# Kernel optimization log

Hardware: AMD Instinct MI355X
Metric: run time of the kernel (lower is better)

Reference implementation:

```python
import jax, jax.numpy as jnp
import numpy as np

BINS = 256
MIN_V = -0.25
MAX_V = 1.25
XSIGMA = 1.0 / float(np.sqrt(2.0 * np.pi))
DELTA = (MAX_V - MIN_V) / BINS
SIGMA = DELTA * XSIGMA
# constant prefactor applied once to the joint kernel: delta / (sqrt(2*pi)*sigma)
COEF = float(DELTA / (np.sqrt(2.0 * np.pi) * SIGMA))

B, N = 8, 32768


def setup_inputs() -> dict:
    key = jax.random.key(0)
    k1, k2, k3 = jax.random.split(key, 3)
    x1 = jax.random.uniform(k1, (B, N), dtype=jnp.float32)
    x2 = jax.random.uniform(k2, (B, N), dtype=jnp.float32)
    mask = jax.random.uniform(k3, (B, N), dtype=jnp.float32)
    return {"x1": x1, "x2": x2, "mask": mask}


def reference(x1, x2, mask):
    # bin centers: (bins,)
    centers = MIN_V + DELTA * (jnp.arange(BINS, dtype=x1.dtype) + 0.5)
    inv_s = 1.0 / SIGMA
    # Separable factorization of exp(-0.5*((x1-ci)^2+(x2-cj)^2)/sigma^2):
    # g1: (b, bins, N), g2: (b, bins, N) with mask folded into g2.
    d1 = (x1[:, None, :] - centers[None, :, None]) * inv_s
    d2 = (x2[:, None, :] - centers[None, :, None]) * inv_s
    g1 = jnp.exp(-0.5 * d1 * d1)
    g2 = jnp.exp(-0.5 * d2 * d2) * mask[:, None, :]
    # contract over N via batched matmul -> (b, bins, bins)
    hist = jnp.einsum("bin,bjn->bij", g1, g2)
    return COEF * hist
```

## Files before the change

### kernel.cpp

```cpp
#include <hip/hip_runtime.h>


#define BINS   256
#define NPTS   32768
#define BATCH  8
#define TROWS  8
#define NTILE  (BINS / TROWS)

static constexpr float kInvDelta = 256.0f / 1.5f;
static constexpr float kUAdd     = 0.25f * (256.0f / 1.5f) - 0.5f;
static constexpr float kPi       = 3.14159265358979323846f;

__global__ __launch_bounds__(1024) void gh_gather(
    const float* __restrict__ x1, const float* __restrict__ x2,
    const float* __restrict__ mask, float* __restrict__ out)
{
    __shared__ float tile[TROWS * BINS];
    const int tid = threadIdx.x;
    const int r0  = blockIdx.x * TROWS;
    const int b   = blockIdx.y;

    for (int i = tid; i < TROWS * BINS; i += 1024) tile[i] = 0.0f;
    __syncthreads();

    const float4* X1 = (const float4*)(x1   + b * NPTS);
    const float4* X2 = (const float4*)(x2   + b * NPTS);
    const float4* M  = (const float4*)(mask + b * NPTS);

#pragma unroll 2
    for (int it = 0; it < NPTS / 4096; ++it) {
        const int n4 = it * 1024 + tid;
        const float4 a4 = X1[n4];
        const float4 b4 = X2[n4];
        const float4 m4 = M[n4];

        const float pv1[4] = {a4.x, a4.y, a4.z, a4.w};
        const float pv2[4] = {b4.x, b4.y, b4.z, b4.w};
        const float pm[4]  = {m4.x, m4.y, m4.z, m4.w};

#pragma unroll
        for (int k = 0; k < 4; ++k) {
            const float u1 = fmaf(pv1[k], kInvDelta, kUAdd);
            const float u2 = fmaf(pv2[k], kInvDelta, kUAdd);
            const float fi = rintf(u1);
            const float fj = rintf(u2);
            const int   i0 = (int)fi;
            int         j0 = (int)fj;
            j0 = min(254, max(1, j0));
            const float t1 = u1 - fi;
            const float t2 = u2 - (float)j0;

            float w1[3], w2[3];
#pragma unroll
            for (int a = 0; a < 3; ++a) {
                const float d1 = t1 - (float)(a - 1);
                const float d2 = t2 - (float)(a - 1);
                w1[a] = __expf(-kPi * d1 * d1);
                w2[a] = __expf(-kPi * d2 * d2) * pm[k];
            }

            const int rbase = i0 - 1 - r0;
            const int cbase = j0 - 1;
#pragma unroll
            for (int a = 0; a < 3; ++a) {
                const int r = rbase + a;
                if ((unsigned)r < TROWS) {
                    const float wa  = w1[a];
                    const int   off = r * BINS + cbase;
                    atomicAdd(&tile[off + 0], wa * w2[0]);
                    atomicAdd(&tile[off + 1], wa * w2[1]);
                    atomicAdd(&tile[off + 2], wa * w2[2]);
                }
            }
        }
    }
    __syncthreads();

    float4*       o4 = (float4*)(out + ((size_t)b * BINS + r0) * BINS);
    const float4* t4 = (const float4*)tile;
    for (int i = tid; i < TROWS * BINS / 4; i += 1024) o4[i] = t4[i];
}

extern "C" void kernel_launch(void* const* d_in, const int* in_sizes, int n_in,
                              void* d_out, int out_size, void* d_ws, size_t ws_size,
                              hipStream_t stream) {
    const float* x1   = (const float*)d_in[0];
    const float* x2   = (const float*)d_in[1];
    const float* mask = (const float*)d_in[2];
    float*       out  = (float*)d_out;

    gh_gather<<<dim3(NTILE, BATCH), 1024, 0, stream>>>(x1, x2, mask, out);
}
```

Baseline: 80.15 us.

## Widen row tiles and split points across blocks with a merge kernel

Each block now owns 32 histogram rows instead of 8 and processes only a quarter of a batch's points. The four partial histograms are written to workspace and summed by a second kernel. Previously every block re-read and re-evaluated Gaussian weights for all points but kept only the few that hit its rows, so this cuts that redundant per-point work about fourfold. The cost is a 2D-to-3D grid change, an extra kernel launch, and extra global traffic for the partial buffers. The weight exponents are also rewritten in expanded quadratic form, and the row index is now clamped like the column index.

```diff
diff --git a/kernel.cpp b/kernel.cpp
--- a/kernel.cpp
+++ b/kernel.cpp
@@ -4,36 +4,41 @@
 #define BINS   256
 #define NPTS   32768
 #define BATCH  8
-#define TROWS  8
+#define TROWS  32
 #define NTILE  (BINS / TROWS)
+#define NSPLIT 4
+#define PPB    (NPTS / NSPLIT)
+#define QSTRIDE (BATCH * BINS * BINS)
 
 static constexpr float kInvDelta = 256.0f / 1.5f;
 static constexpr float kUAdd     = 0.25f * (256.0f / 1.5f) - 0.5f;
 static constexpr float kPi       = 3.14159265358979323846f;
+static constexpr float k2Pi      = 2.0f * kPi;
 
-__global__ __launch_bounds__(1024) void gh_gather(
+__global__ __launch_bounds__(1024) void gh_scatter(
     const float* __restrict__ x1, const float* __restrict__ x2,
-    const float* __restrict__ mask, float* __restrict__ out)
+    const float* __restrict__ mask, float* __restrict__ part)
 {
     __shared__ float tile[TROWS * BINS];
-    const int tid = threadIdx.x;
-    const int r0  = blockIdx.x * TROWS;
-    const int b   = blockIdx.y;
+    const int tid  = threadIdx.x;
+    const int tl   = blockIdx.x;
+    const int q    = blockIdx.y;
+    const int b    = blockIdx.z;
+    const int r0   = tl * TROWS;
 
     for (int i = tid; i < TROWS * BINS; i += 1024) tile[i] = 0.0f;
     __syncthreads();
 
-    const float4* X1 = (const float4*)(x1   + b * NPTS);
-    const float4* X2 = (const float4*)(x2   + b * NPTS);
-    const float4* M  = (const float4*)(mask + b * NPTS);
+    const float4* X1 = (const float4*)(x1   + b * NPTS + q * PPB);
+    const float4* X2 = (const float4*)(x2   + b * NPTS + q * PPB);
+    const float4* M  = (const float4*)(mask + b * NPTS + q * PPB);
 
-#pragma unroll 2
-    for (int it = 0; it < NPTS / 4096; ++it) {
+#pragma unroll
+    for (int it = 0; it < PPB / 4096; ++it) {
         const int n4 = it * 1024 + tid;
         const float4 a4 = X1[n4];
         const float4 b4 = X2[n4];
         const float4 m4 = M[n4];
-
         const float pv1[4] = {a4.x, a4.y, a4.z, a4.w};
         const float pv2[4] = {b4.x, b4.y, b4.z, b4.w};
         const float pm[4]  = {m4.x, m4.y, m4.z, m4.w};
@@ -44,29 +49,31 @@
             const float u2 = fmaf(pv2[k], kInvDelta, kUAdd);
             const float fi = rintf(u1);
             const float fj = rintf(u2);
-            const int   i0 = (int)fi;
-            int         j0 = (int)fj;
+            int i0 = (int)fi, j0 = (int)fj;
+            i0 = min(254, max(1, i0));
             j0 = min(254, max(1, j0));
-            const float t1 = u1 - fi;
+            const float t1 = u1 - (float)i0;
             const float t2 = u2 - (float)j0;
 
-            float w1[3], w2[3];
-#pragma unroll
-            for (int a = 0; a < 3; ++a) {
-                const float d1 = t1 - (float)(a - 1);
-                const float d2 = t2 - (float)(a - 1);
-                w1[a] = __expf(-kPi * d1 * d1);
-                w2[a] = __expf(-kPi * d2 * d2) * pm[k];
-            }
+            const float q1 = -kPi * t1 * t1, r1 = k2Pi * t1;
+            const float q2 = -kPi * t2 * t2, r2 = k2Pi * t2;
+            const float w1m = __expf(q1 - r1 - kPi);
+            const float w10 = __expf(q1);
+            const float w1p = __expf(q1 + r1 - kPi);
+            const float w2m = __expf(q2 - r2 - kPi) * pm[k];
+            const float w20 = __expf(q2)            * pm[k];
+            const float w2p = __expf(q2 + r2 - kPi) * pm[k];
+            const float w1[3] = {w1m, w10, w1p};
+            const float w2[3] = {w2m, w20, w2p};
 
             const int rbase = i0 - 1 - r0;
             const int cbase = j0 - 1;
 #pragma unroll
             for (int a = 0; a < 3; ++a) {
-                const int r = rbase + a;
-                if ((unsigned)r < TROWS) {
+                const int rr = rbase + a;
+                if ((unsigned)rr < TROWS) {
                     const float wa  = w1[a];
-                    const int   off = r * BINS + cbase;
+                    const int   off = rr * BINS + cbase;
                     atomicAdd(&tile[off + 0], wa * w2[0]);
                     atomicAdd(&tile[off + 1], wa * w2[1]);
                     atomicAdd(&tile[off + 2], wa * w2[2]);
@@ -76,9 +83,26 @@
     }
     __syncthreads();
 
-    float4*       o4 = (float4*)(out + ((size_t)b * BINS + r0) * BINS);
+    float4*       o4 = (float4*)(part + (size_t)q * QSTRIDE + b * 65536 + tl * (TROWS * BINS));
     const float4* t4 = (const float4*)tile;
     for (int i = tid; i < TROWS * BINS / 4; i += 1024) o4[i] = t4[i];
+}
+
+__global__ __launch_bounds__(256) void gh_merge(
+    const float* __restrict__ part, float* __restrict__ out)
+{
+    const int i = blockIdx.x * blockDim.x + threadIdx.x;
+    const float4* p4 = (const float4*)part;
+    float4 s0 = p4[i];
+    float4 s1 = p4[i + QSTRIDE / 4];
+    float4 s2 = p4[i + 2 * (QSTRIDE / 4)];
+    float4 s3 = p4[i + 3 * (QSTRIDE / 4)];
+    float4 r;
+    r.x = (s0.x + s1.x) + (s2.x + s3.x);
+    r.y = (s0.y + s1.y) + (s2.y + s3.y);
+    r.z = (s0.z + s1.z) + (s2.z + s3.z);
+    r.w = (s0.w + s1.w) + (s2.w + s3.w);
+    ((float4*)out)[i] = r;
 }
 
 extern "C" void kernel_launch(void* const* d_in, const int* in_sizes, int n_in,
@@ -88,6 +112,8 @@
     const float* x2   = (const float*)d_in[1];
     const float* mask = (const float*)d_in[2];
     float*       out  = (float*)d_out;
+    float*       part = (float*)d_ws;
 
-    gh_gather<<<dim3(NTILE, BATCH), 1024, 0, stream>>>(x1, x2, mask, out);
+    gh_scatter<<<dim3(NTILE, NSPLIT, BATCH), 1024, 0, stream>>>(x1, x2, mask, part);
+    gh_merge<<<(QSTRIDE / 4) / 256, 256, 0, stream>>>(part, out);
 }
```

Measured after the change: 83.19 us. +3.8%, slower.

## Compact relevant points into shared queue before computing weights and scattering

Applied to the files above, without the earlier changes.

Each block first reads only x1 and uses wave ballots to compact the indices of points whose row bin falls near its 8-row tile into a shared queue. It then gathers x2 and mask only for those points and computes the Gaussian weights and atomic adds. This avoids loading x2 and mask and evaluating exponentials for the roughly 29/32 of points that never touch the tile. It also rewrites the three exps per axis from a shared quadratic term. The queue is capped at 6144 entries, so a skewed x1 distribution would silently drop points, and the gather loads are scattered.

```diff
diff --git a/kernel.cpp b/kernel.cpp
--- a/kernel.cpp
+++ b/kernel.cpp
@@ -1,76 +1,104 @@
 #include <hip/hip_runtime.h>
 
 
-#define BINS   256
-#define NPTS   32768
-#define BATCH  8
-#define TROWS  8
-#define NTILE  (BINS / TROWS)
+#define BINS  256
+#define NPTS  32768
+#define BATCH 8
+#define TROWS 8
+#define NTILE (BINS / TROWS)
+#define QMAX  6144
 
 static constexpr float kInvDelta = 256.0f / 1.5f;
 static constexpr float kUAdd     = 0.25f * (256.0f / 1.5f) - 0.5f;
 static constexpr float kPi       = 3.14159265358979323846f;
+static constexpr float k2Pi      = 2.0f * kPi;
 
 __global__ __launch_bounds__(1024) void gh_gather(
     const float* __restrict__ x1, const float* __restrict__ x2,
     const float* __restrict__ mask, float* __restrict__ out)
 {
-    __shared__ float tile[TROWS * BINS];
-    const int tid = threadIdx.x;
-    const int r0  = blockIdx.x * TROWS;
-    const int b   = blockIdx.y;
+    __shared__ float          tile[TROWS * BINS];
+    __shared__ unsigned short queue[QMAX];
+    __shared__ int            qcnt;
+
+    const int tid  = threadIdx.x;
+    const int lane = tid & 63;
+    const int r0   = blockIdx.x * TROWS;
+    const int b    = blockIdx.y;
 
     for (int i = tid; i < TROWS * BINS; i += 1024) tile[i] = 0.0f;
+    if (tid == 0) qcnt = 0;
     __syncthreads();
 
-    const float4* X1 = (const float4*)(x1   + b * NPTS);
-    const float4* X2 = (const float4*)(x2   + b * NPTS);
-    const float4* M  = (const float4*)(mask + b * NPTS);
+    const float4* X1 = (const float4*)(x1 + b * NPTS);
+#pragma unroll
+    for (int it = 0; it < NPTS / 4096; ++it) {
+        const int    n4 = it * 1024 + tid;
+        const float4 a4 = X1[n4];
+        const float  pv[4] = {a4.x, a4.y, a4.z, a4.w};
 
-#pragma unroll 2
-    for (int it = 0; it < NPTS / 4096; ++it) {
-        const int n4 = it * 1024 + tid;
-        const float4 a4 = X1[n4];
-        const float4 b4 = X2[n4];
-        const float4 m4 = M[n4];
-
-        const float pv1[4] = {a4.x, a4.y, a4.z, a4.w};
-        const float pv2[4] = {b4.x, b4.y, b4.z, b4.w};
-        const float pm[4]  = {m4.x, m4.y, m4.z, m4.w};
-
+        bool h[4];
 #pragma unroll
         for (int k = 0; k < 4; ++k) {
-            const float u1 = fmaf(pv1[k], kInvDelta, kUAdd);
-            const float u2 = fmaf(pv2[k], kInvDelta, kUAdd);
-            const float fi = rintf(u1);
-            const float fj = rintf(u2);
-            const int   i0 = (int)fi;
-            int         j0 = (int)fj;
-            j0 = min(254, max(1, j0));
-            const float t1 = u1 - fi;
-            const float t2 = u2 - (float)j0;
+            const float u1 = fmaf(pv[k], kInvDelta, kUAdd);
+            const int   i0 = (int)rintf(u1);
+            h[k] = (unsigned)(i0 - 1 - r0 + 2) < (unsigned)(TROWS + 2);
+        }
+        unsigned long long bal[4];
+        int cnt[4];
+#pragma unroll
+        for (int k = 0; k < 4; ++k) { bal[k] = __ballot(h[k]); cnt[k] = __popcll(bal[k]); }
 
-            float w1[3], w2[3];
+        int wb = 0;
+        if (lane == 0) wb = atomicAdd(&qcnt, cnt[0] + cnt[1] + cnt[2] + cnt[3]);
+        wb = __shfl(wb, 0, 64);
+
+        const unsigned long long below = (lane == 63) ? ~0ull >> 1
+                                       : ((1ull << lane) - 1ull);
+        int run = wb;
 #pragma unroll
-            for (int a = 0; a < 3; ++a) {
-                const float d1 = t1 - (float)(a - 1);
-                const float d2 = t2 - (float)(a - 1);
-                w1[a] = __expf(-kPi * d1 * d1);
-                w2[a] = __expf(-kPi * d2 * d2) * pm[k];
+        for (int k = 0; k < 4; ++k) {
+            if (h[k]) {
+                const int idx = run + __popcll(bal[k] & below);
+                if (idx < QMAX) queue[idx] = (unsigned short)(n4 * 4 + k);
             }
+            run += cnt[k];
+        }
+    }
+    __syncthreads();
 
-            const int rbase = i0 - 1 - r0;
-            const int cbase = j0 - 1;
+    const int qn = min(qcnt, QMAX);
+    const int pbase = b * NPTS;
+    for (int k = tid; k < qn; k += 1024) {
+        const int   n  = queue[k];
+        const float v1 = x1[pbase + n];
+        const float v2 = x2[pbase + n];
+        const float m  = mask[pbase + n];
+
+        const float u1 = fmaf(v1, kInvDelta, kUAdd);
+        const float u2 = fmaf(v2, kInvDelta, kUAdd);
+        const int   i0 = (int)rintf(u1);
+        int         j0 = (int)rintf(u2);
+        j0 = min(254, max(1, j0));
+        const float t1 = u1 - (float)i0;
+        const float t2 = u2 - (float)j0;
+
+        const float e1 = -kPi * t1 * t1, s1 = k2Pi * t1;
+        const float e2 = -kPi * t2 * t2, s2 = k2Pi * t2;
+        const float w1[3] = {__expf(e1 - s1 - kPi), __expf(e1), __expf(e1 + s1 - kPi)};
+        const float w2[3] = {__expf(e2 - s2 - kPi) * m, __expf(e2) * m,
+                             __expf(e2 + s2 - kPi) * m};
+
+        const int rbase = i0 - 1 - r0;
+        const int cbase = j0 - 1;
 #pragma unroll
-            for (int a = 0; a < 3; ++a) {
-                const int r = rbase + a;
-                if ((unsigned)r < TROWS) {
-                    const float wa  = w1[a];
-                    const int   off = r * BINS + cbase;
-                    atomicAdd(&tile[off + 0], wa * w2[0]);
-                    atomicAdd(&tile[off + 1], wa * w2[1]);
-                    atomicAdd(&tile[off + 2], wa * w2[2]);
-                }
+        for (int a = 0; a < 3; ++a) {
+            const int rr = rbase + a;
+            if ((unsigned)rr < TROWS) {
+                const int off = rr * BINS + cbase;
+                atomicAdd(&tile[off + 0], w1[a] * w2[0]);
+                atomicAdd(&tile[off + 1], w1[a] * w2[1]);
+                atomicAdd(&tile[off + 2], w1[a] * w2[2]);
             }
         }
     }
```

After: 82.56 us. 3.0% more time.
